# Optimization experiments

Measured on AMD Instinct MI355X. Metric: run time of the kernel, lower is better.

The kernel has to match this reference:

```python
import jax, jax.numpy as jnp
import numpy as np

EMBED = 1024
HEADS = 16
HEAD_DIM = EMBED // HEADS


def setup_inputs() -> dict:
    key = jax.random.key(0)
    ks = jax.random.split(key, 9)
    s = 0.02
    x = jax.random.normal(ks[0], (2, 2048, EMBED), dtype=jnp.float32)
    Wq = jax.random.normal(ks[1], (EMBED, EMBED), dtype=jnp.float32) * s
    bq = jnp.zeros((EMBED,), dtype=jnp.float32)
    Wk = jax.random.normal(ks[2], (EMBED, EMBED), dtype=jnp.float32) * s
    bk = jnp.zeros((EMBED,), dtype=jnp.float32)
    Wv = jax.random.normal(ks[3], (EMBED, EMBED), dtype=jnp.float32) * s
    bv = jnp.zeros((EMBED,), dtype=jnp.float32)
    Wo = jax.random.normal(ks[4], (EMBED, EMBED), dtype=jnp.float32) * s
    bo = jnp.zeros((EMBED,), dtype=jnp.float32)
    return {"x": x, "Wq": Wq, "bq": bq, "Wk": Wk, "bk": bk,
            "Wv": Wv, "bv": bv, "Wo": Wo, "bo": bo}


def reference(x, Wq, bq, Wk, bk, Wv, bv, Wo, bo):
    B, S, E = x.shape
    H, D = HEADS, HEAD_DIM
    scale = jnp.sqrt(jnp.asarray(D, dtype=x.dtype))
    # projections (torch Linear: y = x @ W.T + b)
    q = (x @ Wq.T + bq).reshape(B, S, H, D).transpose(0, 2, 1, 3)  # [B,H,S,D]
    k = (x @ Wk.T + bk).reshape(B, S, H, D).transpose(0, 2, 1, 3)
    v = (x @ Wv.T + bv).reshape(B, S, H, D).transpose(0, 2, 1, 3)
    scores = jnp.einsum('bhqd,bhkd->bhqk', q, k) / scale  # [B,H,S,S]
    probs = jax.nn.softmax(scores, axis=-1)
    out = jnp.einsum('bhqk,bhkd->bhqd', probs, v)  # [B,H,S,D]
    out = out.transpose(0, 2, 1, 3).reshape(B, S, E)
    return out @ Wo.T + bo
```

## Files before the change

### kernel.cpp

```cpp
#include <hip/hip_runtime.h>
#include <cstddef>

#define EMBED 1024
#define HEADS 16
#define HDIM  64
#define BATCH 2
#define SEQ   2048
#define MTOT  (BATCH*SEQ)

typedef __attribute__((ext_vector_type(8)))  short short8;
typedef __attribute__((ext_vector_type(4)))  float f32x4;
typedef __attribute__((ext_vector_type(16))) float f32x16;

typedef __attribute__((address_space(1))) const unsigned int* gas_u32p;
typedef __attribute__((address_space(3))) unsigned int* las_u32p;

static __device__ __forceinline__ void gload_lds16(const void* g, void* l) {
    __builtin_amdgcn_global_load_lds((gas_u32p)g, (las_u32p)l, 16, 0, 0);
}

static __device__ __forceinline__ unsigned short f2bf(float x) {
    unsigned u = __builtin_bit_cast(unsigned, x);
    unsigned r = (u + 0x7FFFu + ((u >> 16) & 1u)) >> 16;
    return (unsigned short)r;
}

static __device__ __forceinline__ unsigned pk_bf16(float lo, float hi) {
    unsigned r;
    asm("v_cvt_pk_bf16_f32 %0, %1, %2" : "=v"(r) : "v"(lo), "v"(hi));
    return r;
}

static __device__ __forceinline__ void plane32_swap(unsigned &a, unsigned &b) {
    auto r = __builtin_amdgcn_permlane32_swap((int)a, (int)b, false, false);
    a = (unsigned)r[0];
    b = (unsigned)r[1];
}

static __device__ __forceinline__ f32x16 mfma32(short8 a, short8 b, f32x16 c) {
    return __builtin_amdgcn_mfma_f32_32x32x16_bf16(a, b, c, 0, 0, 0);
}

__global__ __launch_bounds__(256)
void conv_all(const float* __restrict__ x,
              const float* __restrict__ Wq, const float* __restrict__ Wk,
              const float* __restrict__ Wv, const float* __restrict__ Wo,
              unsigned short* __restrict__ xh, unsigned short* __restrict__ Wh)
{
    const size_t i = ((size_t)blockIdx.x * 256 + threadIdx.x) * 8;
    const size_t XTOT = (size_t)MTOT * EMBED;
    const float* src;
    unsigned short* dst;
    size_t off;
    if (i < XTOT) {
        src = x; dst = xh; off = i;
    } else {
        size_t j = i - XTOT;
        int sel = (int)(j >> 20);
        off = j & ((1u << 20) - 1);
        src = sel == 0 ? Wq : sel == 1 ? Wk : sel == 2 ? Wv : Wo;
        dst = Wh + ((size_t)sel << 20);
    }
    float4 a = *(const float4*)(src + off);
    float4 b = *(const float4*)(src + off + 4);
    unsigned short o[8] __attribute__((aligned(16)));
    o[0] = f2bf(a.x); o[1] = f2bf(a.y); o[2] = f2bf(a.z); o[3] = f2bf(a.w);
    o[4] = f2bf(b.x); o[5] = f2bf(b.y); o[6] = f2bf(b.z); o[7] = f2bf(b.w);
    *(uint4*)(dst + off) = *(const uint4*)o;
}

__global__ __launch_bounds__(256)
void gemm_qkv_bf16(const unsigned short* __restrict__ A,
                   const unsigned short* __restrict__ Wqh,
                   const unsigned short* __restrict__ Wkh,
                   const unsigned short* __restrict__ Wvh,
                   const float* __restrict__ bq,
                   const float* __restrict__ bk,
                   const float* __restrict__ bv,
                   unsigned short* __restrict__ Qb,
                   unsigned short* __restrict__ Kb,
                   unsigned short* __restrict__ Vt)
{
    __shared__ short As[128 * 64];
    __shared__ short Bs[128 * 64];

    const int tid  = threadIdx.x;
    const int lane = tid & 63;
    const int w    = tid >> 6;
    const int c    = lane & 15;
    const int g    = lane >> 4;
    const int wr   = w >> 1;
    const int wc   = w & 1;

    const int m0   = blockIdx.y * 128;
    const int bxn  = blockIdx.x;
    const int wsel = bxn >> 3;
    const int n0   = (bxn & 7) * 128;

    const unsigned short* W = (wsel == 0) ? Wqh : (wsel == 1) ? Wkh : Wvh;
    const float* bias       = (wsel == 0) ? bq  : (wsel == 1) ? bk  : bv;

    f32x4 acc[4][4] = {};

    for (int k0 = 0; k0 < EMBED; k0 += 64) {
        __syncthreads();
        #pragma unroll
        for (int i = 0; i < 4; ++i) {
            const int slot = w * 256 + i * 64 + lane;
            const int row  = slot >> 3;
            const int chs  = (slot & 7) ^ (row & 7);
            gload_lds16(A + (size_t)(m0 + row) * EMBED + k0 + chs * 8,
                        As + (size_t)(w * 256 + i * 64) * 8);
            gload_lds16(W + (size_t)(n0 + row) * EMBED + k0 + chs * 8,
                        Bs + (size_t)(w * 256 + i * 64) * 8);
        }
        __syncthreads();

        #pragma unroll
        for (int ks = 0; ks < 2; ++ks) {
            short8 af[4], bf[4];
            #pragma unroll
            for (int mi = 0; mi < 4; ++mi) {
                const int row = wr * 64 + mi * 16 + c;
                const int chn = (ks * 4 + g) ^ (row & 7);
                af[mi] = *(const short8*)&As[row * 64 + chn * 8];
            }
            #pragma unroll
            for (int ni = 0; ni < 4; ++ni) {
                const int row = wc * 64 + ni * 16 + c;
                const int chn = (ks * 4 + g) ^ (row & 7);
                bf[ni] = *(const short8*)&Bs[row * 64 + chn * 8];
            }
            #pragma unroll
            for (int mi = 0; mi < 4; ++mi)
                #pragma unroll
                for (int ni = 0; ni < 4; ++ni)
                    acc[mi][ni] = __builtin_amdgcn_mfma_f32_16x16x32_bf16(
                        af[mi], bf[ni], acc[mi][ni], 0, 0, 0);
        }
    }

    if (wsel == 2) {
        #pragma unroll
        for (int mi = 0; mi < 4; ++mi) {
            const int m  = m0 + wr * 64 + mi * 16 + g * 4;
            const int bb = m >> 11;
            const int ss = m & (SEQ - 1);
            #pragma unroll
            for (int ni = 0; ni < 4; ++ni) {
                const int col = n0 + wc * 64 + ni * 16 + c;
                const int hh = col >> 6, dd = col & 63;
                const float bi_ = bias[col];
                ushort4 o;
                o.x = f2bf(acc[mi][ni][0] + bi_);
                o.y = f2bf(acc[mi][ni][1] + bi_);
                o.z = f2bf(acc[mi][ni][2] + bi_);
                o.w = f2bf(acc[mi][ni][3] + bi_);
                *(ushort4*)&Vt[((size_t)((bb * HEADS + hh) * HDIM) + dd) * SEQ + ss] = o;
            }
        }
    } else {
        unsigned short* Out = (wsel == 0) ? Qb : Kb;
        const float oscale  = (wsel == 0) ? 0.180336880f : 1.0f;
        #pragma unroll
        for (int mi = 0; mi < 4; ++mi)
            #pragma unroll
            for (int r = 0; r < 4; ++r) {
                const int m = m0 + wr * 64 + mi * 16 + g * 4 + r;
                #pragma unroll
                for (int ni = 0; ni < 4; ++ni) {
                    const int col = n0 + wc * 64 + ni * 16 + c;
                    Out[(size_t)m * EMBED + col] =
                        f2bf((acc[mi][ni][r] + bias[col]) * oscale);
                }
            }
    }
}

__global__ __launch_bounds__(256)
void gemm_o_bf16(const unsigned short* __restrict__ A,
                 const unsigned short* __restrict__ Woh,
                 const float* __restrict__ bo,
                 float* __restrict__ C)
{
    __shared__ short As[128 * 64];
    __shared__ short Bs[128 * 64];

    const int tid  = threadIdx.x;
    const int lane = tid & 63;
    const int w    = tid >> 6;
    const int c    = lane & 15;
    const int g    = lane >> 4;
    const int wr   = w >> 1;
    const int wc   = w & 1;

    const int m0 = blockIdx.y * 128;
    const int n0 = blockIdx.x * 128;

    f32x4 acc[4][4] = {};

    for (int k0 = 0; k0 < EMBED; k0 += 64) {
        __syncthreads();
        #pragma unroll
        for (int i = 0; i < 4; ++i) {
            const int slot = w * 256 + i * 64 + lane;
            const int row  = slot >> 3;
            const int chs  = (slot & 7) ^ (row & 7);
            gload_lds16(A   + (size_t)(m0 + row) * EMBED + k0 + chs * 8,
                        As + (size_t)(w * 256 + i * 64) * 8);
            gload_lds16(Woh + (size_t)(n0 + row) * EMBED + k0 + chs * 8,
                        Bs + (size_t)(w * 256 + i * 64) * 8);
        }
        __syncthreads();

        #pragma unroll
        for (int ks = 0; ks < 2; ++ks) {
            short8 af[4], bf[4];
            #pragma unroll
            for (int mi = 0; mi < 4; ++mi) {
                const int row = wr * 64 + mi * 16 + c;
                const int chn = (ks * 4 + g) ^ (row & 7);
                af[mi] = *(const short8*)&As[row * 64 + chn * 8];
            }
            #pragma unroll
            for (int ni = 0; ni < 4; ++ni) {
                const int row = wc * 64 + ni * 16 + c;
                const int chn = (ks * 4 + g) ^ (row & 7);
                bf[ni] = *(const short8*)&Bs[row * 64 + chn * 8];
            }
            #pragma unroll
            for (int mi = 0; mi < 4; ++mi)
                #pragma unroll
                for (int ni = 0; ni < 4; ++ni)
                    acc[mi][ni] = __builtin_amdgcn_mfma_f32_16x16x32_bf16(
                        af[mi], bf[ni], acc[mi][ni], 0, 0, 0);
        }
    }

    #pragma unroll
    for (int mi = 0; mi < 4; ++mi)
        #pragma unroll
        for (int r = 0; r < 4; ++r) {
            const int m = m0 + wr * 64 + mi * 16 + g * 4 + r;
            #pragma unroll
            for (int ni = 0; ni < 4; ++ni) {
                const int col = n0 + wc * 64 + ni * 16 + c;
                C[(size_t)m * EMBED + col] = acc[mi][ni][r] + bo[col];
            }
        }
}

__global__ __launch_bounds__(512)
void flash_attn_mfma6(const unsigned short* __restrict__ Qb,
                      const unsigned short* __restrict__ Kb,
                      const unsigned short* __restrict__ Vt,
                      unsigned short* __restrict__ O)
{
    __shared__ short SLDS[32768];
    __shared__ float MLB[4][64];

    const int tid  = threadIdx.x;
    const int lane = tid & 63;
    const int w    = tid >> 6;
    const int qp   = w & 3;
    const int half = w >> 2;
    const int l31  = lane & 31;
    const int hi   = lane >> 5;
    const int rm   = l31 & 7;
    const int q0   = blockIdx.x * 256 + qp * 64;
    const int h    = blockIdx.y;
    const int b    = blockIdx.z;

    short8 qf[2][4];
    #pragma unroll
    for (int sub = 0; sub < 2; ++sub) {
        const unsigned short* qrow =
            Qb + (size_t)(b * SEQ + q0 + sub * 32 + l31) * EMBED + h * HDIM + hi * 8;
        #pragma unroll
        for (int kc = 0; kc < 4; ++kc)
            qf[sub][kc] = *(const short8*)(qrow + kc * 16);
    }

    const int tb     = w >> 1;
    const int sthalf = tb >> 1;
    const int stV    = tb & 1;
    const int ssub   = w & 1;
    const int strow  = ssub * 32 + (lane >> 3);
    const int ch     = (lane & 7) ^ (strow & 7);
    const unsigned short* kS =
        Kb + (size_t)(b * SEQ + sthalf * (SEQ / 2) + strow) * EMBED + h * HDIM + ch * 8;
    const unsigned short* vS =
        Vt + ((size_t)((b * HEADS + h) * HDIM) + strow) * SEQ + sthalf * (SEQ / 2) + ch * 8;

    f32x16 acc[2][2] = {};
    float l_run[2] = {0.f, 0.f};

    #define STAGE(kt2, bb)                                                    \
        do {                                                                  \
            if (stV == 0) {                                                   \
                const unsigned short* src = kS + (size_t)(kt2) * 64 * EMBED;  \
                short* kd = &SLDS[(sthalf * 2 + (bb)) * 4096 + ssub * 2048];  \
                _Pragma("unroll")                                             \
                for (int it = 0; it < 4; ++it)                                \
                    gload_lds16(src + (size_t)it * 8 * EMBED, kd + it * 512); \
            } else {                                                          \
                const unsigned short* src = vS + (kt2) * 64;                  \
                short* vd = &SLDS[16384 + (sthalf * 2 + (bb)) * 4096          \
                                  + ssub * 2048];                            \
                _Pragma("unroll")                                             \
                for (int it = 0; it < 4; ++it)                                \
                    gload_lds16(src + (size_t)it * 8 * SEQ, vd + it * 512);   \
            }                                                                 \
        } while (0)

    STAGE(0, 0);
    __syncthreads();

    for (int kt = 0; kt < SEQ / 2 / 64; ++kt) {
        const int bi = kt & 1;
        if (kt < SEQ / 2 / 64 - 1) STAGE(kt + 1, bi ^ 1);

        const short* kb_ = &SLDS[(half * 2 + bi) * 4096];
        const short* vb_ = &SLDS[16384 + (half * 2 + bi) * 4096];

        short8 ka[2][4];
        #pragma unroll
        for (int t = 0; t < 2; ++t)
            #pragma unroll
            for (int kc = 0; kc < 4; ++kc)
                ka[t][kc] = *(const short8*)
                    &kb_[(t * 32 + l31) * 64 + (((2 * kc + hi) ^ rm) * 8)];

        short8 pf[2][2][2];
        #pragma unroll
        for (int sub = 0; sub < 2; ++sub) {
            f32x16 s[2] = {};
            __builtin_amdgcn_s_setprio(1);
            #pragma unroll
            for (int t = 0; t < 2; ++t)
                #pragma unroll
                for (int kc = 0; kc < 4; ++kc)
                    s[t] = mfma32(ka[t][kc], qf[sub][kc], s[t]);
            __builtin_amdgcn_s_setprio(0);

            float rs = 0.f;
            #pragma unroll
            for (int t = 0; t < 2; ++t)
                #pragma unroll
                for (int r = 0; r < 16; ++r) {
                    float pv = __builtin_amdgcn_exp2f(s[t][r]);
                    s[t][r] = pv;
                    rs += pv;
                }
            l_run[sub] += rs;

            #pragma unroll
            for (int t = 0; t < 2; ++t)
                #pragma unroll
                for (int kc = 0; kc < 2; ++kc) {
                    unsigned A0 = pk_bf16(s[t][8 * kc + 0], s[t][8 * kc + 1]);
                    unsigned A1 = pk_bf16(s[t][8 * kc + 2], s[t][8 * kc + 3]);
                    unsigned B0 = pk_bf16(s[t][8 * kc + 4], s[t][8 * kc + 5]);
                    unsigned B1 = pk_bf16(s[t][8 * kc + 6], s[t][8 * kc + 7]);
                    plane32_swap(A0, B0);
                    plane32_swap(A1, B1);
                    uint4 fw = make_uint4(A0, A1, B0, B1);
                    pf[sub][t][kc] = __builtin_bit_cast(short8, fw);
                }
        }

        __builtin_amdgcn_s_setprio(1);
        #pragma unroll
        for (int dt = 0; dt < 2; ++dt)
            #pragma unroll
            for (int t = 0; t < 2; ++t)
                #pragma unroll
                for (int kc = 0; kc < 2; ++kc) {
                    short8 vf = *(const short8*)
                        &vb_[(dt * 32 + l31) * 64 + (((4 * t + 2 * kc + hi) ^ rm) * 8)];
                    acc[0][dt] = mfma32(pf[0][t][kc], vf, acc[0][dt]);
                    acc[1][dt] = mfma32(pf[1][t][kc], vf, acc[1][dt]);
                }
        __builtin_amdgcn_s_setprio(0);

        __syncthreads();
    }
    #undef STAGE

    float lt[2];
    #pragma unroll
    for (int sub = 0; sub < 2; ++sub)
        lt[sub] = l_run[sub] + __shfl_xor(l_run[sub], 32, 64);

    float* mrgf = (float*)&SLDS[0];
    if (half == 1) {
        #pragma unroll
        for (int sub = 0; sub < 2; ++sub)
            #pragma unroll
            for (int dt = 0; dt < 2; ++dt)
                #pragma unroll
                for (int r = 0; r < 16; ++r) {
                    const int qr = (r & 3) + 8 * (r >> 2) + 4 * hi;
                    mrgf[qp * 4096 + (sub * 32 + qr) * 64 + dt * 32 + l31]
                        = acc[sub][dt][r];
                }
        if (hi == 0) {
            MLB[qp][l31]      = lt[0];
            MLB[qp][l31 + 32] = lt[1];
        }
    }
    __syncthreads();
    if (half == 0) {
        #pragma unroll
        for (int sub = 0; sub < 2; ++sub) {
            const float lo  = MLB[qp][sub * 32 + l31];
            const float inv = 1.f / (lt[sub] + lo);
            #pragma unroll
            for (int r = 0; r < 16; ++r) {
                const int qr = (r & 3) + 8 * (r >> 2) + 4 * hi;
                float invr = __shfl(inv, qr, 64);
                #pragma unroll
                for (int dt = 0; dt < 2; ++dt) {
                    float oh = mrgf[qp * 4096 + (sub * 32 + qr) * 64 + dt * 32 + l31];
                    float val = (acc[sub][dt][r] + oh) * invr;
                    O[(size_t)(b * SEQ + q0 + sub * 32 + qr) * EMBED
                      + h * HDIM + dt * 32 + l31] = f2bf(val);
                }
            }
        }
    }
}

extern "C" void kernel_launch(void* const* d_in, const int* in_sizes, int n_in,
                              void* d_out, int out_size, void* d_ws, size_t ws_size,
                              hipStream_t stream)
{
    const float* x  = (const float*)d_in[0];
    const float* Wq = (const float*)d_in[1];
    const float* bq = (const float*)d_in[2];
    const float* Wk = (const float*)d_in[3];
    const float* bk = (const float*)d_in[4];
    const float* Wv = (const float*)d_in[5];
    const float* bv = (const float*)d_in[6];
    const float* Wo = (const float*)d_in[7];
    const float* bo = (const float*)d_in[8];
    float* out = (float*)d_out;

    const size_t ME = (size_t)MTOT * EMBED;
    unsigned short* xh   = (unsigned short*)d_ws;
    unsigned short* Qb   = xh   + ME;
    unsigned short* Kb   = Qb   + ME;
    unsigned short* Vt   = Kb   + ME;
    unsigned short* attn = Vt   + ME;
    unsigned short* Wh   = attn + ME;

    dim3 blk(256);

    conv_all<<<dim3((2 * ME) / 2048), blk, 0, stream>>>(x, Wq, Wk, Wv, Wo, xh, Wh);

    gemm_qkv_bf16<<<dim3(24, MTOT / 128), blk, 0, stream>>>(
        xh, Wh, Wh + (size_t)EMBED * EMBED, Wh + 2 * (size_t)EMBED * EMBED,
        bq, bk, bv, Qb, Kb, Vt);

    flash_attn_mfma6<<<dim3(SEQ / 256, HEADS, BATCH), dim3(512), 0, stream>>>(
        Qb, Kb, Vt, attn);

    gemm_o_bf16<<<dim3(EMBED / 128, MTOT / 128), blk, 0, stream>>>(
        attn, Wh + 3 * (size_t)EMBED * EMBED, bo, out);
}
```

Measured before the change: 123.7 us.

## Split attention KV range four ways per block with 128-query tiles

The flash attention kernel now uses 128 queries per block instead of 256, and each block's eight waves become 2 query groups times 4 KV quarters of 512 keys each. The grid doubles, aiming for more blocks and better CU occupancy. Each wave group loads its own KV quarter with a single-buffered load followed by syncs, replacing the double-buffered prefetch, so there is less overlap of loads with compute. A two-stage LDS tree reduction merges the four partial outputs and their softmax denominators, adding epilogue work and extra barriers.

```diff
diff --git a/kernel.cpp b/kernel.cpp
--- a/kernel.cpp
+++ b/kernel.cpp
@@ -251,23 +251,23 @@
 }
 
 __global__ __launch_bounds__(512)
-void flash_attn_mfma6(const unsigned short* __restrict__ Qb,
+void flash_attn_mfma7(const unsigned short* __restrict__ Qb,
                       const unsigned short* __restrict__ Kb,
                       const unsigned short* __restrict__ Vt,
                       unsigned short* __restrict__ O)
 {
     __shared__ short SLDS[32768];
-    __shared__ float MLB[4][64];
+    __shared__ float MLB[2][2][64];
 
     const int tid  = threadIdx.x;
     const int lane = tid & 63;
     const int w    = tid >> 6;
-    const int qp   = w & 3;
-    const int half = w >> 2;
+    const int qp   = w & 1;
+    const int qr4  = w >> 1;
     const int l31  = lane & 31;
     const int hi   = lane >> 5;
     const int rm   = l31 & 7;
-    const int q0   = blockIdx.x * 256 + qp * 64;
+    const int q0   = blockIdx.x * 128 + qp * 64;
     const int h    = blockIdx.y;
     const int b    = blockIdx.z;
 
@@ -281,47 +281,34 @@
             qf[sub][kc] = *(const short8*)(qrow + kc * 16);
     }
 
-    const int tb     = w >> 1;
-    const int sthalf = tb >> 1;
-    const int stV    = tb & 1;
-    const int ssub   = w & 1;
-    const int strow  = ssub * 32 + (lane >> 3);
-    const int ch     = (lane & 7) ^ (strow & 7);
-    const unsigned short* kS =
-        Kb + (size_t)(b * SEQ + sthalf * (SEQ / 2) + strow) * EMBED + h * HDIM + ch * 8;
-    const unsigned short* vS =
-        Vt + ((size_t)((b * HEADS + h) * HDIM) + strow) * SEQ + sthalf * (SEQ / 2) + ch * 8;
+    const int srow = lane >> 3;
+    const int sch  = (lane & 7) ^ srow;
+    const unsigned short* gs;
+    size_t it_step, kt_step;
+    if (qp == 0) {
+        gs = Kb + (size_t)(b * SEQ + qr4 * 512 + srow) * EMBED + h * HDIM + sch * 8;
+        it_step = (size_t)8 * EMBED;
+        kt_step = (size_t)64 * EMBED;
+    } else {
+        gs = Vt + ((size_t)((b * HEADS + h) * HDIM) + srow) * SEQ + qr4 * 512 + sch * 8;
+        it_step = (size_t)8 * SEQ;
+        kt_step = (size_t)64;
+    }
+    short* sdst = &SLDS[(qp ? 16384 : 0) + qr4 * 4096];
+
+    const short* kb_ = &SLDS[qr4 * 4096];
+    const short* vb_ = &SLDS[16384 + qr4 * 4096];
 
     f32x16 acc[2][2] = {};
     float l_run[2] = {0.f, 0.f};
 
-    #define STAGE(kt2, bb)                                                    \
-        do {                                                                  \
-            if (stV == 0) {                                                   \
-                const unsigned short* src = kS + (size_t)(kt2) * 64 * EMBED;  \
-                short* kd = &SLDS[(sthalf * 2 + (bb)) * 4096 + ssub * 2048];  \
-                _Pragma("unroll")                                             \
-                for (int it = 0; it < 4; ++it)                                \
-                    gload_lds16(src + (size_t)it * 8 * EMBED, kd + it * 512); \
-            } else {                                                          \
-                const unsigned short* src = vS + (kt2) * 64;                  \
-                short* vd = &SLDS[16384 + (sthalf * 2 + (bb)) * 4096          \
-                                  + ssub * 2048];                            \
-                _Pragma("unroll")                                             \
-                for (int it = 0; it < 4; ++it)                                \
-                    gload_lds16(src + (size_t)it * 8 * SEQ, vd + it * 512);   \
-            }                                                                 \
-        } while (0)
-
-    STAGE(0, 0);
-    __syncthreads();
-
-    for (int kt = 0; kt < SEQ / 2 / 64; ++kt) {
-        const int bi = kt & 1;
-        if (kt < SEQ / 2 / 64 - 1) STAGE(kt + 1, bi ^ 1);
-
-        const short* kb_ = &SLDS[(half * 2 + bi) * 4096];
-        const short* vb_ = &SLDS[16384 + (half * 2 + bi) * 4096];
+    for (int kt = 0; kt < 8; ++kt) {
+        __syncthreads();
+        #pragma unroll
+        for (int it = 0; it < 8; ++it)
+            gload_lds16(gs + (size_t)it * it_step, sdst + it * 512);
+        gs += kt_step;
+        __syncthreads();
 
         short8 ka[2][4];
         #pragma unroll
@@ -382,10 +369,7 @@
                     acc[1][dt] = mfma32(pf[1][t][kc], vf, acc[1][dt]);
                 }
         __builtin_amdgcn_s_setprio(0);
-
-        __syncthreads();
-    }
-    #undef STAGE
+    }
 
     float lt[2];
     #pragma unroll
@@ -393,7 +377,43 @@
         lt[sub] = l_run[sub] + __shfl_xor(l_run[sub], 32, 64);
 
     float* mrgf = (float*)&SLDS[0];
-    if (half == 1) {
+
+    __syncthreads();
+    if (qr4 & 1) {
+        float* M = mrgf + (qr4 >> 1) * 8192;
+        #pragma unroll
+        for (int sub = 0; sub < 2; ++sub)
+            #pragma unroll
+            for (int dt = 0; dt < 2; ++dt)
+                #pragma unroll
+                for (int r = 0; r < 16; ++r) {
+                    const int qr = (r & 3) + 8 * (r >> 2) + 4 * hi;
+                    M[qp * 4096 + (sub * 32 + qr) * 64 + dt * 32 + l31]
+                        = acc[sub][dt][r];
+                }
+        if (hi == 0) {
+            MLB[qr4 >> 1][qp][l31]      = lt[0];
+            MLB[qr4 >> 1][qp][l31 + 32] = lt[1];
+        }
+    }
+    __syncthreads();
+    if (!(qr4 & 1)) {
+        const float* M = mrgf + (qr4 >> 1) * 8192;
+        #pragma unroll
+        for (int sub = 0; sub < 2; ++sub) {
+            lt[sub] += MLB[qr4 >> 1][qp][sub * 32 + l31];
+            #pragma unroll
+            for (int dt = 0; dt < 2; ++dt)
+                #pragma unroll
+                for (int r = 0; r < 16; ++r) {
+                    const int qr = (r & 3) + 8 * (r >> 2) + 4 * hi;
+                    acc[sub][dt][r] +=
+                        M[qp * 4096 + (sub * 32 + qr) * 64 + dt * 32 + l31];
+                }
+        }
+    }
+    __syncthreads();
+    if (qr4 == 2) {
         #pragma unroll
         for (int sub = 0; sub < 2; ++sub)
             #pragma unroll
@@ -405,15 +425,15 @@
                         = acc[sub][dt][r];
                 }
         if (hi == 0) {
-            MLB[qp][l31]      = lt[0];
-            MLB[qp][l31 + 32] = lt[1];
+            MLB[0][qp][l31]      = lt[0];
+            MLB[0][qp][l31 + 32] = lt[1];
         }
     }
     __syncthreads();
-    if (half == 0) {
+    if (qr4 == 0) {
         #pragma unroll
         for (int sub = 0; sub < 2; ++sub) {
-            const float lo  = MLB[qp][sub * 32 + l31];
+            const float lo  = MLB[0][qp][sub * 32 + l31];
             const float inv = 1.f / (lt[sub] + lo);
             #pragma unroll
             for (int r = 0; r < 16; ++r) {
@@ -462,7 +482,7 @@
         xh, Wh, Wh + (size_t)EMBED * EMBED, Wh + 2 * (size_t)EMBED * EMBED,
         bq, bk, bv, Qb, Kb, Vt);
 
-    flash_attn_mfma6<<<dim3(SEQ / 256, HEADS, BATCH), dim3(512), 0, stream>>>(
+    flash_attn_mfma7<<<dim3(SEQ / 128, HEADS, BATCH), dim3(512), 0, stream>>>(
         Qb, Kb, Vt, attn);
 
     gemm_o_bf16<<<dim3(EMBED / 128, MTOT / 128), blk, 0, stream>>>(
```

New measurement: 136.4 us. 1.1x slower.
